# Performance work log

Measured on AMD Instinct MI355X. Metric: run time of the kernel, lower is better.

Reference implementation:

```python
import jax, jax.numpy as jnp
import numpy as np

M, F_IN, F_OUT, K = 8192, 32, 32, 5


def setup_inputs() -> dict:
    key = jax.random.key(0)
    k1, k2, k3 = jax.random.split(key, 3)
    x = jax.random.normal(k1, (M, F_IN), dtype=jnp.float32)
    # scale so spectral radius ~O(1); real simplicial Laplacians have bounded spectrum
    L = jax.random.normal(k2, (M, M), dtype=jnp.float32) / jnp.sqrt(jnp.float32(M))
    # xavier-uniform-like scale for W (gain for relu)
    gain = jnp.sqrt(jnp.float32(2.0))
    bound = gain * jnp.sqrt(jnp.float32(6.0 / (F_IN + F_OUT)))
    W = jax.random.uniform(k3, (K, F_IN, F_OUT), dtype=jnp.float32,
                           minval=-bound, maxval=bound)
    return {"x": x, "L": L, "W": W}


def reference(x, L, W):
    """y = sum_{k=0}^{K-1} L^k @ x @ W[k].

    Math identical to the torch module, but computed via the recursive
    propagation z_k = L @ z_{k-1} (z_0 = x), i.e. O(K*M^2*F) instead of
    forming dense matrix powers L^k (O(K*M^3)).
    """
    y0 = x @ W[0]                      # [M, F_out], k = 0 term (L^0 = I)

    def body(z, Wk):
        z = L @ z                      # z_k = L @ z_{k-1}, [M, F_in]
        return z, z @ Wk               # term_k = L^k x W[k], [M, F_out]

    _, terms = jax.lax.scan(body, x, W[1:])   # terms: [K-1, M, F_out]
    return y0 + terms.sum(axis=0)
```

## Files before the change

### kernel.cpp

```cpp
#include <hip/hip_runtime.h>

typedef unsigned short u16;
typedef unsigned int u32;
typedef __bf16 bf16x8 __attribute__((ext_vector_type(8)));
typedef float f32x4 __attribute__((ext_vector_type(4)));
typedef u32 u32x2 __attribute__((ext_vector_type(2)));
typedef u32 u32x4 __attribute__((ext_vector_type(4)));

#define M_DIM 8192
#define CCH 512
#define NCH (M_DIM / CCH)

__device__ __forceinline__ u16 f2bf(float f) {
  return __builtin_bit_cast(u16, (__bf16)f);
}

union Frag {
  bf16x8 f;
  u16 s[8];
  u32x2 h2[2];
  u32x4 q;
};


__global__ __launch_bounds__(256) void head_kernel(
    const float* __restrict__ x, const float* __restrict__ W0,
    float* __restrict__ y_out, u16* __restrict__ zbt0) {
  __shared__ float Ws[1024];
  __shared__ u16 zsb[256][34];
  const int t = threadIdx.x;
  for (int i = t; i < 1024; i += 256) Ws[i] = W0[i];
  const int m = blockIdx.x * 256 + t;
  float z[32];
  const float4* xr = (const float4*)(x + (size_t)m * 32);
#pragma unroll
  for (int i = 0; i < 8; i++) {
    float4 v = xr[i];
    z[4 * i] = v.x; z[4 * i + 1] = v.y; z[4 * i + 2] = v.z; z[4 * i + 3] = v.w;
  }
#pragma unroll
  for (int c = 0; c < 32; c++) zsb[t][c] = f2bf(z[c]);
  __syncthreads();
  float acc[32];
#pragma unroll
  for (int j = 0; j < 32; j++) acc[j] = 0.f;
#pragma unroll
  for (int c = 0; c < 32; c++) {
#pragma unroll
    for (int j = 0; j < 32; j++) acc[j] += z[c] * Ws[c * 32 + j];
  }
  float4* yo = (float4*)(y_out + (size_t)m * 32);
#pragma unroll
  for (int i = 0; i < 8; i++) {
    float4 v; v.x = acc[4 * i]; v.y = acc[4 * i + 1];
    v.z = acc[4 * i + 2]; v.w = acc[4 * i + 3];
    yo[i] = v;
  }
  const int lane = t & 63, w = t >> 6;
  const int l15 = lane & 15, l4 = lane >> 4;
#pragma unroll
  for (int i = 0; i < 4; i++) {
    int tile = w * 4 + i;
    int ktl = tile >> 1, nt = tile & 1;
    Frag fr;
#pragma unroll
    for (int j = 0; j < 8; j++) fr.s[j] = zsb[ktl * 32 + 8 * l4 + j][nt * 16 + l15];
    size_t kt_g = (size_t)blockIdx.x * 8 + ktl;
    *(u32x4*)(zbt0 + ((kt_g * 2 + nt) * 64 + lane) * 8) = fr.q;
  }
}

__global__ __launch_bounds__(512, 4) void conv_kernel(
    const float* __restrict__ L, const u16* __restrict__ zbt0,
    const float* __restrict__ W1, const float* __restrict__ y_in,
    float* __restrict__ y_out, u16* __restrict__ Lbt,
    u16* __restrict__ zbt_out) {
  __shared__ u16 At[2][16][520];
  __shared__ float red[8][16][33];
  __shared__ float Ws[1024];
  __shared__ float zs[16][33];
  __shared__ u16 zsb[16][36];
  const int t = threadIdx.x;
  const int lane = t & 63, w = t >> 6;
  const int l15 = lane & 15, l4 = lane >> 4;
  const int bx = blockIdx.x;
  const int r0 = bx * 16;
  for (int i = t; i < 1024; i += 512) Ws[i] = W1[i];

  const int srow = t >> 5, scg = t & 31;
  const float* sbase = L + (size_t)(r0 + srow) * M_DIM + scg * 4;

  auto stage = [&](int c, int buf) {
    const float* src = sbase + c * CCH;
    u16* dst = &At[buf][srow][scg * 4];
#pragma unroll
    for (int seg = 0; seg < 4; seg++) {
      f32x4 v = __builtin_nontemporal_load((const f32x4*)(src + seg * 128));
      u32x2 p;
      p[0] = (u32)f2bf(v[0]) | ((u32)f2bf(v[1]) << 16);
      p[1] = (u32)f2bf(v[2]) | ((u32)f2bf(v[3]) << 16);
      *(u32x2*)(dst + seg * 128) = p;
    }
  };

  f32x4 acc0 = {0.f, 0.f, 0.f, 0.f};
  f32x4 acc1 = {0.f, 0.f, 0.f, 0.f};

  stage(0, 0);
  int buf = 0;
  for (int c = 0; c < NCH; c++) {
    __syncthreads();
    if (c + 1 < NCH) stage(c + 1, buf ^ 1);
#pragma unroll
    for (int i = 0; i < 2; i++) {
      const int ktl = c * 16 + w * 2 + i;
      Frag fa;
      fa.q = *(const u32x4*)&At[buf][l15][(w * 2 + i) * 32 + 8 * l4];
      *(u32x4*)(Lbt + ((size_t)bx * 256 + ktl) * 512 + lane * 8) = fa.q;
      Frag fb0, fb1;
      size_t bo = ((size_t)ktl * 2) * 512 + lane * 8;
      fb0.q = *(const u32x4*)(zbt0 + bo);
      fb1.q = *(const u32x4*)(zbt0 + bo + 512);
      acc0 = __builtin_amdgcn_mfma_f32_16x16x32_bf16(fa.f, fb0.f, acc0, 0, 0, 0);
      acc1 = __builtin_amdgcn_mfma_f32_16x16x32_bf16(fa.f, fb1.f, acc1, 0, 0, 0);
    }
    buf ^= 1;
  }

#pragma unroll
  for (int r = 0; r < 4; r++) {
    red[w][4 * l4 + r][l15] = acc0[r];
    red[w][4 * l4 + r][l15 + 16] = acc1[r];
  }
  __syncthreads();
  const int row = t >> 5, j = t & 31;
  float v = 0.f;
#pragma unroll
  for (int s = 0; s < 8; s++) v += red[s][row][j];
  zs[row][j] = v;
  zsb[row][j] = f2bf(v);
  __syncthreads();
  float yv = y_in[(size_t)(r0 + row) * 32 + j];
#pragma unroll
  for (int c = 0; c < 32; c++) yv += zs[row][c] * Ws[c * 32 + j];
  y_out[(size_t)(r0 + row) * 32 + j] = yv;

  if (t < 64) {
    const int nt = t >> 5, li = t & 31;
    const int kt = bx >> 1, h = bx & 1;
    Frag fr;
#pragma unroll
    for (int jj = 0; jj < 8; jj++)
      fr.s[jj] = zsb[8 * (li >> 4) + jj][nt * 16 + (li & 15)];
    *(u32x4*)(zbt_out + (size_t)((kt * 2 + nt) * 64 + 32 * h + li) * 8) = fr.q;
  }
}

template <bool LAST>
__global__ __launch_bounds__(512, 4) void fpass_kernel(
    const u16* __restrict__ Lbt, const u16* __restrict__ zbt,
    const float* __restrict__ Wk, const float* __restrict__ y_in,
    float* __restrict__ y_out, u16* __restrict__ zbt_out) {
  __shared__ float red[8][16][33];
  __shared__ float Ws[1024];
  __shared__ float zs[16][33];
  __shared__ u16 zsb[16][36];
  const int t = threadIdx.x;
  const int lane = t & 63, w = t >> 6;
  const int l15 = lane & 15, l4 = lane >> 4;
  const int bx = blockIdx.x;
  for (int i = t; i < 1024; i += 512) Ws[i] = Wk[i];

  const u16* ap = Lbt + ((size_t)bx * 256 + w * 32) * 512 + lane * 8;
  const u16* bp = zbt + (size_t)(w * 32) * 1024 + lane * 8;

  f32x4 acc0 = {0.f, 0.f, 0.f, 0.f};
  f32x4 acc1 = {0.f, 0.f, 0.f, 0.f};
#pragma unroll 8
  for (int kt = 0; kt < 32; kt++) {
    Frag fa, fb0, fb1;
    fa.q = *(const u32x4*)(ap + (size_t)kt * 512);
    fb0.q = *(const u32x4*)(bp + (size_t)kt * 1024);
    fb1.q = *(const u32x4*)(bp + (size_t)kt * 1024 + 512);
    acc0 = __builtin_amdgcn_mfma_f32_16x16x32_bf16(fa.f, fb0.f, acc0, 0, 0, 0);
    acc1 = __builtin_amdgcn_mfma_f32_16x16x32_bf16(fa.f, fb1.f, acc1, 0, 0, 0);
  }
#pragma unroll
  for (int r = 0; r < 4; r++) {
    red[w][4 * l4 + r][l15] = acc0[r];
    red[w][4 * l4 + r][l15 + 16] = acc1[r];
  }
  __syncthreads();
  const int row = t >> 5, j = t & 31;
  float v = 0.f;
#pragma unroll
  for (int s = 0; s < 8; s++) v += red[s][row][j];
  zs[row][j] = v;
  zsb[row][j] = f2bf(v);
  __syncthreads();
  float yv = y_in[(size_t)(bx * 16 + row) * 32 + j];
#pragma unroll
  for (int c = 0; c < 32; c++) yv += zs[row][c] * Ws[c * 32 + j];
  y_out[(size_t)(bx * 16 + row) * 32 + j] = yv;

  if (!LAST && t < 64) {
    const int nt = t >> 5, li = t & 31;
    const int kt = bx >> 1, h = bx & 1;
    Frag fr;
#pragma unroll
    for (int jj = 0; jj < 8; jj++)
      fr.s[jj] = zsb[8 * (li >> 4) + jj][nt * 16 + (li & 15)];
    *(u32x4*)(zbt_out + (size_t)((kt * 2 + nt) * 64 + 32 * h + li) * 8) = fr.q;
  }
}

extern "C" void kernel_launch(void* const* d_in, const int* in_sizes, int n_in,
                              void* d_out, int out_size, void* d_ws,
                              size_t ws_size, hipStream_t stream) {
  const float* x = (const float*)d_in[0];
  const float* L = (const float*)d_in[1];
  const float* W = (const float*)d_in[2];
  float* y = (float*)d_out;
  char* ws = (char*)d_ws;

  const size_t ZT = (size_t)512 << 10;
  u16* zbt0 = (u16*)(ws + 0 * ZT);
  u16* zbt1 = (u16*)(ws + 1 * ZT);
  u16* zbt2 = (u16*)(ws + 2 * ZT);
  u16* zbt3 = (u16*)(ws + 3 * ZT);
  float* y_acc = (float*)(ws + ((size_t)10 << 20));
  u16* Lbt = (u16*)(ws + ((size_t)12 << 20));

  head_kernel<<<32, 256, 0, stream>>>(x, W, y_acc, zbt0);
  conv_kernel<<<512, 512, 0, stream>>>(L, zbt0, W + 1024, y_acc, y_acc, Lbt, zbt1);
  fpass_kernel<false><<<512, 512, 0, stream>>>(Lbt, zbt1, W + 2048, y_acc, y_acc, zbt2);
  fpass_kernel<false><<<512, 512, 0, stream>>>(Lbt, zbt2, W + 3072, y_acc, y_acc, zbt3);
  fpass_kernel<true><<<512, 512, 0, stream>>>(Lbt, zbt3, W + 4096, y_acc, y, (u16*)0);
}
```

Measured before the change: 174.5 us.

## Split L conversion into standalone bandwidth kernel and run first hop as fpass

The fused conv kernel, which converted L to a bf16 MFMA tile layout while computing the first propagation hop, becomes a pure streaming conversion kernel with 8192 blocks and no LDS or MFMA work. The first hop then runs through the existing fpass kernel on the converted Lbt. The aim is to let the dominant 256 MB fp32 read of L run at full bandwidth without double buffering, LDS staging and syncs. In exchange there is one extra launch and an extra 128 MB read of Lbt for the first hop.

```diff
diff --git a/kernel.cpp b/kernel.cpp
--- a/kernel.cpp
+++ b/kernel.cpp
@@ -8,8 +8,6 @@
 typedef u32 u32x4 __attribute__((ext_vector_type(4)));
 
 #define M_DIM 8192
-#define CCH 512
-#define NCH (M_DIM / CCH)
 
 __device__ __forceinline__ u16 f2bf(float f) {
   return __builtin_bit_cast(u16, (__bf16)f);
@@ -70,89 +68,37 @@
   }
 }
 
-__global__ __launch_bounds__(512, 4) void conv_kernel(
-    const float* __restrict__ L, const u16* __restrict__ zbt0,
-    const float* __restrict__ W1, const float* __restrict__ y_in,
-    float* __restrict__ y_out, u16* __restrict__ Lbt,
-    u16* __restrict__ zbt_out) {
-  __shared__ u16 At[2][16][520];
-  __shared__ float red[8][16][33];
-  __shared__ float Ws[1024];
-  __shared__ float zs[16][33];
-  __shared__ u16 zsb[16][36];
-  const int t = threadIdx.x;
-  const int lane = t & 63, w = t >> 6;
-  const int l15 = lane & 15, l4 = lane >> 4;
-  const int bx = blockIdx.x;
-  const int r0 = bx * 16;
-  for (int i = t; i < 1024; i += 512) Ws[i] = W1[i];
+__global__ __launch_bounds__(256) void conv_kernel(
+    const float* __restrict__ L, u16* __restrict__ Lbt) {
+  const int gid = blockIdx.x * 256 + threadIdx.x;
+  const int cg = gid & 1023;
+  const int rg = gid >> 10;
+  const int c = cg * 8;
+  const int r = rg * 4;
+  const int rt = r >> 4;
+  const int ktile = c >> 5;
+  const int q = (c & 31) >> 3;
+  const float* src = L + (size_t)r * M_DIM + c;
+  u16* dst = Lbt + ((size_t)rt * 256 + ktile) * 512 + ((r & 15) + 16 * q) * 8;
 
-  const int srow = t >> 5, scg = t & 31;
-  const float* sbase = L + (size_t)(r0 + srow) * M_DIM + scg * 4;
-
-  auto stage = [&](int c, int buf) {
-    const float* src = sbase + c * CCH;
-    u16* dst = &At[buf][srow][scg * 4];
+  f32x4 v[4][2];
 #pragma unroll
-    for (int seg = 0; seg < 4; seg++) {
-      f32x4 v = __builtin_nontemporal_load((const f32x4*)(src + seg * 128));
-      u32x2 p;
-      p[0] = (u32)f2bf(v[0]) | ((u32)f2bf(v[1]) << 16);
-      p[1] = (u32)f2bf(v[2]) | ((u32)f2bf(v[3]) << 16);
-      *(u32x2*)(dst + seg * 128) = p;
-    }
-  };
-
-  f32x4 acc0 = {0.f, 0.f, 0.f, 0.f};
-  f32x4 acc1 = {0.f, 0.f, 0.f, 0.f};
-
-  stage(0, 0);
-  int buf = 0;
-  for (int c = 0; c < NCH; c++) {
-    __syncthreads();
-    if (c + 1 < NCH) stage(c + 1, buf ^ 1);
+  for (int i = 0; i < 4; i++) {
+    const float* sr = src + (size_t)i * M_DIM;
+    v[i][0] = __builtin_nontemporal_load((const f32x4*)sr);
+    v[i][1] = __builtin_nontemporal_load((const f32x4*)(sr + 4));
+  }
 #pragma unroll
-    for (int i = 0; i < 2; i++) {
-      const int ktl = c * 16 + w * 2 + i;
-      Frag fa;
-      fa.q = *(const u32x4*)&At[buf][l15][(w * 2 + i) * 32 + 8 * l4];
-      *(u32x4*)(Lbt + ((size_t)bx * 256 + ktl) * 512 + lane * 8) = fa.q;
-      Frag fb0, fb1;
-      size_t bo = ((size_t)ktl * 2) * 512 + lane * 8;
-      fb0.q = *(const u32x4*)(zbt0 + bo);
-      fb1.q = *(const u32x4*)(zbt0 + bo + 512);
-      acc0 = __builtin_amdgcn_mfma_f32_16x16x32_bf16(fa.f, fb0.f, acc0, 0, 0, 0);
-      acc1 = __builtin_amdgcn_mfma_f32_16x16x32_bf16(fa.f, fb1.f, acc1, 0, 0, 0);
-    }
-    buf ^= 1;
-  }
-
-#pragma unroll
-  for (int r = 0; r < 4; r++) {
-    red[w][4 * l4 + r][l15] = acc0[r];
-    red[w][4 * l4 + r][l15 + 16] = acc1[r];
-  }
-  __syncthreads();
-  const int row = t >> 5, j = t & 31;
-  float v = 0.f;
-#pragma unroll
-  for (int s = 0; s < 8; s++) v += red[s][row][j];
-  zs[row][j] = v;
-  zsb[row][j] = f2bf(v);
-  __syncthreads();
-  float yv = y_in[(size_t)(r0 + row) * 32 + j];
-#pragma unroll
-  for (int c = 0; c < 32; c++) yv += zs[row][c] * Ws[c * 32 + j];
-  y_out[(size_t)(r0 + row) * 32 + j] = yv;
-
-  if (t < 64) {
-    const int nt = t >> 5, li = t & 31;
-    const int kt = bx >> 1, h = bx & 1;
+  for (int i = 0; i < 4; i++) {
     Frag fr;
 #pragma unroll
-    for (int jj = 0; jj < 8; jj++)
-      fr.s[jj] = zsb[8 * (li >> 4) + jj][nt * 16 + (li & 15)];
-    *(u32x4*)(zbt_out + (size_t)((kt * 2 + nt) * 64 + 32 * h + li) * 8) = fr.q;
+    for (int h = 0; h < 2; h++) {
+      fr.s[4 * h + 0] = f2bf(v[i][h][0]);
+      fr.s[4 * h + 1] = f2bf(v[i][h][1]);
+      fr.s[4 * h + 2] = f2bf(v[i][h][2]);
+      fr.s[4 * h + 3] = f2bf(v[i][h][3]);
+    }
+    *(u32x4*)(dst + i * 8) = fr.q;
   }
 }
 
@@ -232,7 +178,8 @@
   u16* Lbt = (u16*)(ws + ((size_t)12 << 20));
 
   head_kernel<<<32, 256, 0, stream>>>(x, W, y_acc, zbt0);
-  conv_kernel<<<512, 512, 0, stream>>>(L, zbt0, W + 1024, y_acc, y_acc, Lbt, zbt1);
+  conv_kernel<<<8192, 256, 0, stream>>>(L, Lbt);
+  fpass_kernel<false><<<512, 512, 0, stream>>>(Lbt, zbt0, W + 1024, y_acc, y_acc, zbt1);
   fpass_kernel<false><<<512, 512, 0, stream>>>(Lbt, zbt1, W + 2048, y_acc, y_acc, zbt2);
   fpass_kernel<false><<<512, 512, 0, stream>>>(Lbt, zbt2, W + 3072, y_acc, y_acc, zbt3);
   fpass_kernel<true><<<512, 512, 0, stream>>>(Lbt, zbt3, W + 4096, y_acc, y, (u16*)0);
```

Result: slower. 227.0 us (+30.1%).

## Stage L chunks via direct global-to-LDS loads and convert to bf16 at fragment read

Applied to the files above, without the earlier changes.

The conv kernel now streams fp32 L rows straight into shared memory with global_load_lds in 256-column chunks, instead of loading into registers, converting to bf16 and writing to LDS. The bf16 conversion moves to the point where each wave reads its MFMA fragment. The reduction buffer now aliases the staging buffer, and the occupancy hint rises to 6 blocks per SM. The goal is to cut register pressure and VALU work on the HBM-bound first pass over L and raise memory-level parallelism. The cost is one barrier per chunk at twice as many chunks, plus fp32 LDS traffic.

```diff
diff --git a/kernel.cpp b/kernel.cpp
--- a/kernel.cpp
+++ b/kernel.cpp
@@ -8,8 +8,9 @@
 typedef u32 u32x4 __attribute__((ext_vector_type(4)));
 
 #define M_DIM 8192
-#define CCH 512
+#define CCH 256
 #define NCH (M_DIM / CCH)
+#define ROWU 260
 
 __device__ __forceinline__ u16 f2bf(float f) {
   return __builtin_bit_cast(u16, (__bf16)f);
@@ -70,16 +71,16 @@
   }
 }
 
-__global__ __launch_bounds__(512, 4) void conv_kernel(
+__global__ __launch_bounds__(512, 6) void conv_kernel(
     const float* __restrict__ L, const u16* __restrict__ zbt0,
     const float* __restrict__ W1, const float* __restrict__ y_in,
     float* __restrict__ y_out, u16* __restrict__ Lbt,
     u16* __restrict__ zbt_out) {
-  __shared__ u16 At[2][16][520];
-  __shared__ float red[8][16][33];
+  __shared__ __align__(16) u32 Af[2][16 * ROWU];
   __shared__ float Ws[1024];
   __shared__ float zs[16][33];
   __shared__ u16 zsb[16][36];
+  float (*red)[16][33] = (float (*)[16][33]) & Af[0][0];
   const int t = threadIdx.x;
   const int lane = t & 63, w = t >> 6;
   const int l15 = lane & 15, l4 = lane >> 4;
@@ -87,19 +88,15 @@
   const int r0 = bx * 16;
   for (int i = t; i < 1024; i += 512) Ws[i] = W1[i];
 
-  const int srow = t >> 5, scg = t & 31;
-  const float* sbase = L + (size_t)(r0 + srow) * M_DIM + scg * 4;
-
-  auto stage = [&](int c, int buf) {
-    const float* src = sbase + c * CCH;
-    u16* dst = &At[buf][srow][scg * 4];
-#pragma unroll
-    for (int seg = 0; seg < 4; seg++) {
-      f32x4 v = __builtin_nontemporal_load((const f32x4*)(src + seg * 128));
-      u32x2 p;
-      p[0] = (u32)f2bf(v[0]) | ((u32)f2bf(v[1]) << 16);
-      p[1] = (u32)f2bf(v[2]) | ((u32)f2bf(v[3]) << 16);
-      *(u32x2*)(dst + seg * 128) = p;
+  auto stage = [&](int c, int b) {
+#pragma unroll
+    for (int rr = 0; rr < 2; rr++) {
+      const int r = w * 2 + rr;
+      const float* src = L + (size_t)(r0 + r) * M_DIM + c * CCH + lane * 4;
+      u32* dst = &Af[b][r * ROWU + lane * 4];
+      __builtin_amdgcn_global_load_lds(
+          (const __attribute__((address_space(1))) u32*)src,
+          (__attribute__((address_space(3))) u32*)dst, 16, 0, 0);
     }
   };
 
@@ -107,15 +104,20 @@
   f32x4 acc1 = {0.f, 0.f, 0.f, 0.f};
 
   stage(0, 0);
+  __syncthreads();
   int buf = 0;
   for (int c = 0; c < NCH; c++) {
-    __syncthreads();
     if (c + 1 < NCH) stage(c + 1, buf ^ 1);
-#pragma unroll
-    for (int i = 0; i < 2; i++) {
-      const int ktl = c * 16 + w * 2 + i;
+    {
+      const int ktl = c * 8 + w;
+      const u32* arow = &Af[buf][l15 * ROWU + w * 32 + 8 * l4];
+      f32x4 a0 = *(const f32x4*)arow;
+      f32x4 a1 = *(const f32x4*)(arow + 4);
       Frag fa;
-      fa.q = *(const u32x4*)&At[buf][l15][(w * 2 + i) * 32 + 8 * l4];
+      fa.s[0] = f2bf(a0[0]); fa.s[1] = f2bf(a0[1]);
+      fa.s[2] = f2bf(a0[2]); fa.s[3] = f2bf(a0[3]);
+      fa.s[4] = f2bf(a1[0]); fa.s[5] = f2bf(a1[1]);
+      fa.s[6] = f2bf(a1[2]); fa.s[7] = f2bf(a1[3]);
       *(u32x4*)(Lbt + ((size_t)bx * 256 + ktl) * 512 + lane * 8) = fa.q;
       Frag fb0, fb1;
       size_t bo = ((size_t)ktl * 2) * 512 + lane * 8;
@@ -124,6 +126,7 @@
       acc0 = __builtin_amdgcn_mfma_f32_16x16x32_bf16(fa.f, fb0.f, acc0, 0, 0, 0);
       acc1 = __builtin_amdgcn_mfma_f32_16x16x32_bf16(fa.f, fb1.f, acc1, 0, 0, 0);
     }
+    __syncthreads();
     buf ^= 1;
   }
 
```

Result: slower. 191.9 us (+10.0%).
